# Kernel tuning notes

Hardware: AMD Instinct MI355X
Metric: run time of the kernel (lower is better)

Reference implementation:

```python
import jax, jax.numpy as jnp
import numpy as np

IN, OUT, HID = 64, 32, 256
B, T = 64, 256
NOISE_STD, TAU = 0.05, 0.2


def setup_inputs() -> dict:
    key = jax.random.key(0)
    ks = jax.random.split(key, 8)
    u = jax.random.normal(ks[0], (B, T, IN), dtype=jnp.float32)
    x0 = jax.random.normal(ks[1], (B, HID), dtype=jnp.float32)
    noise = jax.random.normal(ks[2], (T, B, HID), dtype=jnp.float32)
    w_hh_rnn = jax.random.normal(ks[3], (HID, HID), dtype=jnp.float32) * (0.1 / HID ** 0.5)
    w_hh_tbrnn = jax.random.normal(ks[4], (HID, HID, HID), dtype=jnp.float32) * (0.1 / HID)
    w_in_w = jax.random.normal(ks[5], (HID, IN), dtype=jnp.float32)
    w_in_b = jnp.zeros((HID,), dtype=jnp.float32)
    w_out_w = jax.random.normal(ks[6], (OUT, HID), dtype=jnp.float32) * 4.0
    w_out_b = jax.random.normal(ks[7], (OUT,), dtype=jnp.float32) * 0.0
    return {"u": u, "x0": x0, "noise": noise, "w_hh_rnn": w_hh_rnn,
            "w_hh_tbrnn": w_hh_tbrnn, "w_in_w": w_in_w, "w_in_b": w_in_b,
            "w_out_w": w_out_w, "w_out_b": w_out_b}


def reference(u, x0, noise, w_hh_rnn, w_hh_tbrnn, w_in_w, w_in_b, w_out_w, w_out_b):
    # mode='cont', form='rate', adv=False, nonlinearity=tanh, output_nonlinearity=tanh
    u_t_first = jnp.transpose(u, (1, 0, 2))  # [T, B, IN]

    def step(x, inp):
        u_t, n_t = inp
        r = jnp.tanh(x)                                   # rate form
        input_I = u_t @ w_in_w.T + w_in_b                 # [B, HID]
        hidden_W1 = r @ w_hh_rnn.T                        # [B, HID]
        # out[b,j] = sum_{i,k} r[b,i] * W[j,i,k] * r[b,k]
        hidden_W2 = jnp.einsum('bi,jik,bk->bj', r, w_hh_tbrnn, r)
        rec_x = hidden_W1 + hidden_W2 + input_I
        x_new = x + NOISE_STD * n_t + TAU * (-x + rec_x)  # cont mode
        return x_new, x_new

    x_final, traj = jax.lax.scan(step, x0, (u_t_first, noise))
    trajectories = jnp.transpose(traj, (1, 0, 2))         # [B, T, HID]
    output = jnp.tanh(trajectories) @ w_out_w.T + w_out_b  # [B, T, OUT]
    return output, x_final, trajectories
```

## Files before the change

### kernel.cpp

```cpp
#include <hip/hip_runtime.h>
#include <hip/hip_bf16.h>
#include <math.h>

#define HID 256
#define BSZ 64
#define TLEN 256
#define INW 64
#define OUTW 32
#define NOISE_STD 0.05f
#define TAU 0.2f

typedef __attribute__((ext_vector_type(8))) short short8;
typedef __attribute__((ext_vector_type(4))) float floatx4;
typedef unsigned long long u64;

__device__ __forceinline__ int ridx(int b, int k) {
    int P = ((b >> 2) & 7) ^ ((b & 3) << 1);
    return b * 256 + ((((k >> 3) ^ P) & 31) << 3) + (k & 7);
}

__global__ __launch_bounds__(256) void swizzle_kernel(const float* __restrict__ W,
                                                      __hip_bfloat16* __restrict__ Wsw) {
    int g = blockIdx.x * 256 + threadIdx.x;
    int l  = g & 63;
    int ni = (g >> 6) & 15;
    int kk = (g >> 10) & 7;
    int j  = g >> 13;
    int i  = ni * 16 + (l & 15);
    int k0 = kk * 32 + (l >> 4) * 8;
    const float* __restrict__ src = W + ((size_t)j * HID + i) * HID + k0;
    __hip_bfloat16* __restrict__ dst = Wsw + (size_t)g * 8;
#pragma unroll
    for (int e = 0; e < 8; ++e) dst[e] = __float2bfloat16(src[e]);
}

__global__ __launch_bounds__(256) void init_kernel(const float* __restrict__ x0,
                                                   __hip_bfloat16* __restrict__ rT0) {
    int idx = blockIdx.x * 256 + threadIdx.x;
    int b = idx >> 8, k = idx & 255;
    rT0[k * BSZ + b] = __float2bfloat16(tanhf(x0[idx]));
}

__global__ __launch_bounds__(256) void pre_kernel(const float* __restrict__ u,
                                                  const float* __restrict__ w_in_w,
                                                  const float* __restrict__ w_in_b,
                                                  const float* __restrict__ noise,
                                                  float* __restrict__ pre) {
    __shared__ float ulds[BSZ][INW + 4];
    const int t = blockIdx.x;
    const int j = threadIdx.x;
    {
        int b = threadIdx.x >> 2, q = threadIdx.x & 3;
#pragma unroll
        for (int e = 0; e < 4; ++e) {
            float4 v = *(const float4*)(u + ((size_t)b * TLEN + t) * INW + q * 16 + e * 4);
            *(float4*)&ulds[b][q * 16 + e * 4] = v;
        }
    }
    float wreg[INW];
#pragma unroll
    for (int q = 0; q < INW / 4; ++q) {
        float4 v = *(const float4*)(w_in_w + (size_t)j * INW + q * 4);
        wreg[q * 4 + 0] = v.x; wreg[q * 4 + 1] = v.y;
        wreg[q * 4 + 2] = v.z; wreg[q * 4 + 3] = v.w;
    }
    float bias = w_in_b[j];
    __syncthreads();
    for (int b = 0; b < BSZ; ++b) {
        float s = bias;
#pragma unroll
        for (int in_ = 0; in_ < INW; ++in_) s = fmaf(ulds[b][in_], wreg[in_], s);
        float nz = noise[((size_t)t * BSZ + b) * HID + j];
        pre[((size_t)t * HID + j) * BSZ + b] = NOISE_STD * nz + TAU * s;
    }
}

__global__ __launch_bounds__(256, 1) void persist_kernel(
    const __hip_bfloat16* __restrict__ Wsw,
    const float* __restrict__ w_hh,
    const float* __restrict__ u,
    const float* __restrict__ w_in_w,
    const float* __restrict__ w_in_b,
    const float* __restrict__ noise,
    const float* __restrict__ x0,
    u64* __restrict__ rT0,
    u64* __restrict__ rT1,
    float* __restrict__ traj,
    float* __restrict__ trajWS,
    float* __restrict__ xfinal,
    int* __restrict__ ready,
    const float* __restrict__ pre,
    int use_pre, int use_tws) {
    __shared__ short Wlds[65536];
    __shared__ short rlds[16384];

    const int tid  = threadIdx.x;
    const int j    = blockIdx.x;
    const int w    = tid >> 6;
    const int lane = tid & 63;
    const int quad = lane >> 4;
    const int col  = lane & 15;

    float* redw = (float*)rlds;
    __hip_bfloat16* exch = (__hip_bfloat16*)(rlds + 512);
    u64* exchU = (u64*)(rlds + 512);

    {
        const short* __restrict__ src = (const short*)Wsw + (size_t)j * 65536;
#pragma unroll
        for (int m = 0; m < 32; ++m) {
            int i8 = m * 256 + tid;
            *(short8*)&Wlds[i8 * 8] = *(const short8*)&src[(size_t)i8 * 8];
        }
    }
    float whh_reg[4];
#pragma unroll
    for (int nj = 0; nj < 4; ++nj)
        whh_reg[nj] = w_hh[j * HID + (w * 4 + nj) * 16 + col];

    float xb = 0.f;
    if (tid < BSZ) xb = x0[tid * HID + j];
    __syncthreads();

    const int fill_k = tid >> 4;
    const int fill_b0 = (tid & 15) * 4;

#pragma unroll 1
    for (int t = 0; t < TLEN; ++t) {
        if (t > 0) {
            while (__hip_atomic_load(ready + tid * 16, __ATOMIC_RELAXED,
                                     __HIP_MEMORY_SCOPE_AGENT) < t)
                __builtin_amdgcn_s_sleep(1);
            asm volatile("" ::: "memory");
            __syncthreads();
        }

        const u64* __restrict__ rcur = (t & 1) ? rT1 : rT0;
        u64* __restrict__ rnxt = (t & 1) ? rT0 : rT1;

        float extra = 0.f;
        if (tid < BSZ) {
            if (use_pre) {
                extra = pre[((size_t)t * HID + j) * BSZ + tid];
            } else {
                float isum = w_in_b[j];
                const float4* __restrict__ urow =
                    (const float4*)(u + ((size_t)tid * TLEN + t) * INW);
                const float4* __restrict__ wrow = (const float4*)(w_in_w + (size_t)j * INW);
#pragma unroll
                for (int q = 0; q < INW / 4; ++q) {
                    float4 uu = urow[q], ww = wrow[q];
                    isum = fmaf(uu.x, ww.x, isum);
                    isum = fmaf(uu.y, ww.y, isum);
                    isum = fmaf(uu.z, ww.z, isum);
                    isum = fmaf(uu.w, ww.w, isum);
                }
                float nz = noise[((size_t)t * BSZ + tid) * HID + j];
                extra = NOISE_STD * nz + TAU * isum;
            }
        }

        {
            u64 v[16];
#pragma unroll
            for (int c = 0; c < 16; ++c)
                v[c] = __hip_atomic_load(rcur + c * 256 + tid, __ATOMIC_RELAXED,
                                         __HIP_MEMORY_SCOPE_AGENT);
#pragma unroll
            for (int c = 0; c < 16; ++c) {
                int k = c * 16 + fill_k;
#pragma unroll
                for (int i2 = 0; i2 < 4; ++i2)
                    rlds[ridx(fill_b0 + i2, k)] = (short)(v[c] >> (16 * i2));
            }
        }
        __syncthreads();

        floatx4 acc[4][4];
#pragma unroll
        for (int mb = 0; mb < 4; ++mb)
#pragma unroll
            for (int nj = 0; nj < 4; ++nj) acc[mb][nj] = (floatx4){0.f, 0.f, 0.f, 0.f};

#pragma unroll
        for (int kk = 0; kk < 8; ++kk) {
            short8 afrag[4];
#pragma unroll
            for (int mb = 0; mb < 4; ++mb)
                afrag[mb] = *(const short8*)&rlds[ridx(mb * 16 + col, kk * 32 + quad * 8)];
#pragma unroll
            for (int nj = 0; nj < 4; ++nj) {
                short8 bfrag = *(const short8*)&Wlds[((kk * 16 + (w * 4 + nj)) * 64 + lane) * 8];
#pragma unroll
                for (int mb = 0; mb < 4; ++mb)
                    acc[mb][nj] = __builtin_amdgcn_mfma_f32_16x16x32_bf16(
                        afrag[mb], bfrag, acc[mb][nj], 0, 0, 0);
            }
        }

        float part[16];
#pragma unroll
        for (int p = 0; p < 16; ++p) part[p] = 0.f;

#pragma unroll
        for (int nj = 0; nj < 4; ++nj) {
            int i = (w * 4 + nj) * 16 + col;
            float whh = whh_reg[nj];
#pragma unroll
            for (int mb = 0; mb < 4; ++mb) {
#pragma unroll
                for (int reg = 0; reg < 4; ++reg) {
                    int b = mb * 16 + quad * 4 + reg;
                    short rs = rlds[ridx(b, i)];
                    float rv = __bfloat162float(*(__hip_bfloat16*)&rs);
                    part[mb * 4 + reg] = fmaf(rv, acc[mb][nj][reg] + whh, part[mb * 4 + reg]);
                }
            }
        }
#pragma unroll
        for (int s = 1; s < 16; s <<= 1) {
#pragma unroll
            for (int p = 0; p < 16; ++p) part[p] += __shfl_xor(part[p], s, 64);
        }
        __syncthreads();
        if (col == 0) {
#pragma unroll
            for (int mb = 0; mb < 4; ++mb)
#pragma unroll
                for (int reg = 0; reg < 4; ++reg)
                    redw[w * 64 + mb * 16 + quad * 4 + reg] = part[mb * 4 + reg];
        }
        __syncthreads();

        float xn = 0.f;
        if (tid < BSZ) {
            const int b = tid;
            float rec = redw[b] + redw[64 + b] + redw[128 + b] + redw[192 + b];
            xn = xb + extra + TAU * (rec - xb);
            xb = xn;
            if (use_tws) trajWS[((size_t)t * HID + j) * BSZ + b] = xn;
            if (t < TLEN - 1) exch[b] = __float2bfloat16(tanhf(xn));
        }

        if (t < TLEN - 1) {
            if (tid < 16) {
                u64 pv = exchU[tid];
                __hip_atomic_store(rnxt + j * 16 + tid, pv, __ATOMIC_RELAXED,
                                   __HIP_MEMORY_SCOPE_AGENT);
            }
            if (tid < 64)
                asm volatile("s_waitcnt vmcnt(0)" ::: "memory");
            if (tid == 0)
                __hip_atomic_store(ready + j * 16, t + 1, __ATOMIC_RELAXED,
                                   __HIP_MEMORY_SCOPE_AGENT);
        }

        if (!use_tws && tid < BSZ) {
            traj[((size_t)tid * TLEN + t) * HID + j] = xn;
            if (t == TLEN - 1) xfinal[tid * HID + j] = xn;
        }
        if (use_tws && t == TLEN - 1 && tid < BSZ) {
        }
    }
}

__global__ __launch_bounds__(256) void fixup_kernel(
    const float* __restrict__ trajWS,
    const float* __restrict__ w_out_w,
    const float* __restrict__ w_out_b,
    float* __restrict__ traj,
    float* __restrict__ xfinal,
    float* __restrict__ out) {
    __shared__ float xv[BSZ * 257];
    __shared__ float wol[OUTW * 257];
    const int t = blockIdx.x, tid = threadIdx.x;

#pragma unroll
    for (int it = 0; it < 16; ++it) {
        int flat = it * 1024 + tid * 4;
        float4 v = *(const float4*)(trajWS + (size_t)t * 16384 + flat);
        int jj = flat >> 6, b = flat & 63;
        xv[(b + 0) * 257 + jj] = v.x;
        xv[(b + 1) * 257 + jj] = v.y;
        xv[(b + 2) * 257 + jj] = v.z;
        xv[(b + 3) * 257 + jj] = v.w;
    }
#pragma unroll
    for (int it = 0; it < 8; ++it) {
        int flat = it * 1024 + tid * 4;
        float4 v = *(const float4*)(w_out_w + flat);
        int o = flat >> 8, h = flat & 255;
        *(float4*)&wol[o * 257 + h] = v;
    }
    __syncthreads();

    for (int b = 0; b < BSZ; ++b)
        traj[((size_t)b * TLEN + t) * HID + tid] = xv[b * 257 + tid];
    if (t == TLEN - 1)
        for (int b = 0; b < BSZ; ++b)
            xfinal[b * HID + tid] = xv[b * 257 + tid];

    __syncthreads();
#pragma unroll
    for (int it = 0; it < 64; ++it) {
        int b = it;
        xv[b * 257 + tid] = tanhf(xv[b * 257 + tid]);
    }
    __syncthreads();

    const int o = tid & 31;
    const float bias = w_out_b[o];
#pragma unroll 1
    for (int rep = 0; rep < 8; ++rep) {
        int b = rep * 8 + (tid >> 5);
        float s = bias;
#pragma unroll 8
        for (int h = 0; h < HID; ++h)
            s = fmaf(xv[b * 257 + h], wol[o * 257 + h], s);
        out[((size_t)b * TLEN + t) * OUTW + o] = s;
    }
}

__global__ __launch_bounds__(256) void output_kernel(
    const float* __restrict__ traj, const float* __restrict__ w_out_w,
    const float* __restrict__ w_out_b, float* __restrict__ out) {
    __shared__ float th[8][HID + 1];
    const int bt0 = blockIdx.x * 8;
    const int tid = threadIdx.x;
#pragma unroll
    for (int m = 0; m < 8; ++m) {
        int idx = m * 256 + tid;
        th[idx >> 8][idx & 255] = tanhf(traj[(size_t)bt0 * HID + idx]);
    }
    __syncthreads();
    const int row = tid >> 5, o = tid & 31;
    const float* __restrict__ wrow = w_out_w + (size_t)o * HID;
    float s = w_out_b[o];
#pragma unroll 8
    for (int h = 0; h < HID; ++h) s = fmaf(th[row][h], wrow[h], s);
    out[(size_t)(bt0 + row) * OUTW + o] = s;
}

extern "C" void kernel_launch(void* const* d_in, const int* in_sizes, int n_in,
                              void* d_out, int out_size, void* d_ws, size_t ws_size,
                              hipStream_t stream) {
    const float* u       = (const float*)d_in[0];
    const float* x0      = (const float*)d_in[1];
    const float* noise   = (const float*)d_in[2];
    const float* w_hh    = (const float*)d_in[3];
    const float* W       = (const float*)d_in[4];
    const float* w_in_w  = (const float*)d_in[5];
    const float* w_in_b  = (const float*)d_in[6];
    const float* w_out_w = (const float*)d_in[7];
    const float* w_out_b = (const float*)d_in[8];

    float* out    = (float*)d_out;
    float* xfinal = out + (size_t)BSZ * TLEN * OUTW;
    float* traj   = xfinal + (size_t)BSZ * HID;

    char* ws = (char*)d_ws;
    __hip_bfloat16* Wsw = (__hip_bfloat16*)ws;
    u64*   rT0 = (u64*)(ws + 33554432);
    u64*   rT1 = (u64*)(ws + 33587200);
    int*   rdy = (int*)(ws + 33619968);
    float* tws = (float*)(ws + 33636352);
    float* pre = (float*)(ws + 50413568);
    const size_t NEED_TWS = 50413568ull;
    const size_t NEED_PRE = 67190784ull;
    const int use_tws = (ws_size >= NEED_TWS) ? 1 : 0;
    const int use_pre = (ws_size >= NEED_PRE) ? 1 : 0;

    hipMemsetAsync(rdy, 0, 16384, stream);
    swizzle_kernel<<<8192, 256, 0, stream>>>(W, Wsw);
    init_kernel<<<64, 256, 0, stream>>>(x0, (__hip_bfloat16*)rT0);
    if (use_pre)
        pre_kernel<<<TLEN, 256, 0, stream>>>(u, w_in_w, w_in_b, noise, pre);

    persist_kernel<<<256, 256, 0, stream>>>(
        Wsw, w_hh, u, w_in_w, w_in_b, noise, x0,
        rT0, rT1, traj, tws, xfinal, rdy, pre, use_pre, use_tws);

    if (use_tws)
        fixup_kernel<<<TLEN, 256, 0, stream>>>(tws, w_out_w, w_out_b, traj, xfinal, out);
    else
        output_kernel<<<(BSZ * TLEN) / 8, 256, 0, stream>>>(traj, w_out_w, w_out_b, out);
}
```

Baseline: 1.759 ms.

## Replace ready-flag barrier with sequence-tagged data packets and register-resident weights

Drops the separate per-block ready counter and its store/fence/spin handshake. Each exchanged 64-bit word now carries three bf16 rates plus a 16-bit timestep tag, so consumers poll the data itself until every tag matches the current step. The per-block 128KB weight slice also moves from LDS into 32 short8 registers per thread, which frees shared memory but raises register pressure substantially. The tagged scheme relies on each 64-bit atomic store being seen whole; buffer layout and the init kernel change to match the new packet format.

New measurement: 2.848 ms. 1.62x slower.

```diff
diff --git a/kernel.cpp b/kernel.cpp
--- a/kernel.cpp
+++ b/kernel.cpp
@@ -9,6 +9,7 @@
 #define OUTW 32
 #define NOISE_STD 0.05f
 #define TAU 0.2f
+#define NPKT 22
 
 typedef __attribute__((ext_vector_type(8))) short short8;
 typedef __attribute__((ext_vector_type(4))) float floatx4;
@@ -35,10 +36,19 @@
 }
 
 __global__ __launch_bounds__(256) void init_kernel(const float* __restrict__ x0,
-                                                   __hip_bfloat16* __restrict__ rT0) {
-    int idx = blockIdx.x * 256 + threadIdx.x;
-    int b = idx >> 8, k = idx & 255;
-    rT0[k * BSZ + b] = __float2bfloat16(tanhf(x0[idx]));
+                                                   u64* __restrict__ buf0) {
+    int c = blockIdx.x;
+    int k = threadIdx.x;
+    u64 v = 0;
+#pragma unroll
+    for (int e = 0; e < 3; ++e) {
+        int b = 3 * c + e;
+        if (b < BSZ) {
+            __hip_bfloat16 h = __float2bfloat16(tanhf(x0[b * HID + k]));
+            v |= (u64)(*(unsigned short*)&h) << (16 * e);
+        }
+    }
+    buf0[c * 256 + k] = v;
 }
 
 __global__ __launch_bounds__(256) void pre_kernel(const float* __restrict__ u,
@@ -83,16 +93,16 @@
     const float* __restrict__ w_in_b,
     const float* __restrict__ noise,
     const float* __restrict__ x0,
-    u64* __restrict__ rT0,
-    u64* __restrict__ rT1,
+    u64* __restrict__ buf0,
+    u64* __restrict__ buf1,
     float* __restrict__ traj,
     float* __restrict__ trajWS,
     float* __restrict__ xfinal,
-    int* __restrict__ ready,
     const float* __restrict__ pre,
     int use_pre, int use_tws) {
-    __shared__ short Wlds[65536];
     __shared__ short rlds[16384];
+    __shared__ float redw[256];
+    __shared__ __hip_bfloat16 exch[BSZ];
 
     const int tid  = threadIdx.x;
     const int j    = blockIdx.x;
@@ -101,17 +111,15 @@
     const int quad = lane >> 4;
     const int col  = lane & 15;
 
-    float* redw = (float*)rlds;
-    __hip_bfloat16* exch = (__hip_bfloat16*)(rlds + 512);
-    u64* exchU = (u64*)(rlds + 512);
-
+    short8 wreg[32];
     {
-        const short* __restrict__ src = (const short*)Wsw + (size_t)j * 65536;
-#pragma unroll
-        for (int m = 0; m < 32; ++m) {
-            int i8 = m * 256 + tid;
-            *(short8*)&Wlds[i8 * 8] = *(const short8*)&src[(size_t)i8 * 8];
-        }
+        const short* __restrict__ wsh = (const short*)Wsw;
+#pragma unroll
+        for (int kk = 0; kk < 8; ++kk)
+#pragma unroll
+            for (int nj = 0; nj < 4; ++nj)
+                wreg[kk * 4 + nj] = *(const short8*)(wsh +
+                    ((((size_t)j * 8 + kk) * 16 + (w * 4 + nj)) * 64 + lane) * 8);
     }
     float whh_reg[4];
 #pragma unroll
@@ -120,23 +128,11 @@
 
     float xb = 0.f;
     if (tid < BSZ) xb = x0[tid * HID + j];
-    __syncthreads();
-
-    const int fill_k = tid >> 4;
-    const int fill_b0 = (tid & 15) * 4;
 
 #pragma unroll 1
     for (int t = 0; t < TLEN; ++t) {
-        if (t > 0) {
-            while (__hip_atomic_load(ready + tid * 16, __ATOMIC_RELAXED,
-                                     __HIP_MEMORY_SCOPE_AGENT) < t)
-                __builtin_amdgcn_s_sleep(1);
-            asm volatile("" ::: "memory");
-            __syncthreads();
-        }
-
-        const u64* __restrict__ rcur = (t & 1) ? rT1 : rT0;
-        u64* __restrict__ rnxt = (t & 1) ? rT0 : rT1;
+        const u64* __restrict__ rcur = (t & 1) ? buf1 : buf0;
+        u64* __restrict__ rnxt = (t & 1) ? buf0 : buf1;
 
         float extra = 0.f;
         if (tid < BSZ) {
@@ -160,20 +156,30 @@
             }
         }
 
+        u64 v[NPKT];
         {
-            u64 v[16];
-#pragma unroll
-            for (int c = 0; c < 16; ++c)
-                v[c] = __hip_atomic_load(rcur + c * 256 + tid, __ATOMIC_RELAXED,
-                                         __HIP_MEMORY_SCOPE_AGENT);
-#pragma unroll
-            for (int c = 0; c < 16; ++c) {
-                int k = c * 16 + fill_k;
-#pragma unroll
-                for (int i2 = 0; i2 < 4; ++i2)
-                    rlds[ridx(fill_b0 + i2, k)] = (short)(v[c] >> (16 * i2));
+            unsigned need = (1u << NPKT) - 1;
+            while (need) {
+#pragma unroll
+                for (int c = 0; c < NPKT; ++c)
+                    if (need & (1u << c))
+                        v[c] = __hip_atomic_load(rcur + c * 256 + tid, __ATOMIC_RELAXED,
+                                                 __HIP_MEMORY_SCOPE_AGENT);
+#pragma unroll
+                for (int c = 0; c < NPKT; ++c)
+                    if ((need & (1u << c)) && (unsigned)(v[c] >> 48) == (unsigned)t)
+                        need &= ~(1u << c);
+                if (need) __builtin_amdgcn_s_sleep(1);
             }
         }
+        __syncthreads();
+
+#pragma unroll
+        for (int c = 0; c < NPKT - 1; ++c)
+#pragma unroll
+            for (int e = 0; e < 3; ++e)
+                rlds[ridx(3 * c + e, tid)] = (short)(v[c] >> (16 * e));
+        rlds[ridx(63, tid)] = (short)v[NPKT - 1];
         __syncthreads();
 
         floatx4 acc[4][4];
@@ -189,25 +195,22 @@
             for (int mb = 0; mb < 4; ++mb)
                 afrag[mb] = *(const short8*)&rlds[ridx(mb * 16 + col, kk * 32 + quad * 8)];
 #pragma unroll
-            for (int nj = 0; nj < 4; ++nj) {
-                short8 bfrag = *(const short8*)&Wlds[((kk * 16 + (w * 4 + nj)) * 64 + lane) * 8];
+            for (int nj = 0; nj < 4; ++nj)
 #pragma unroll
                 for (int mb = 0; mb < 4; ++mb)
                     acc[mb][nj] = __builtin_amdgcn_mfma_f32_16x16x32_bf16(
-                        afrag[mb], bfrag, acc[mb][nj], 0, 0, 0);
-            }
+                        afrag[mb], wreg[kk * 4 + nj], acc[mb][nj], 0, 0, 0);
         }
 
         float part[16];
 #pragma unroll
         for (int p = 0; p < 16; ++p) part[p] = 0.f;
-
 #pragma unroll
         for (int nj = 0; nj < 4; ++nj) {
             int i = (w * 4 + nj) * 16 + col;
             float whh = whh_reg[nj];
 #pragma unroll
-            for (int mb = 0; mb < 4; ++mb) {
+            for (int mb = 0; mb < 4; ++mb)
 #pragma unroll
                 for (int reg = 0; reg < 4; ++reg) {
                     int b = mb * 16 + quad * 4 + reg;
@@ -215,14 +218,12 @@
                     float rv = __bfloat162float(*(__hip_bfloat16*)&rs);
                     part[mb * 4 + reg] = fmaf(rv, acc[mb][nj][reg] + whh, part[mb * 4 + reg]);
                 }
-            }
         }
 #pragma unroll
         for (int s = 1; s < 16; s <<= 1) {
 #pragma unroll
             for (int p = 0; p < 16; ++p) part[p] += __shfl_xor(part[p], s, 64);
         }
-        __syncthreads();
         if (col == 0) {
 #pragma unroll
             for (int mb = 0; mb < 4; ++mb)
@@ -234,32 +235,28 @@
 
         float xn = 0.f;
         if (tid < BSZ) {
-            const int b = tid;
-            float rec = redw[b] + redw[64 + b] + redw[128 + b] + redw[192 + b];
+            float rec = redw[tid] + redw[64 + tid] + redw[128 + tid] + redw[192 + tid];
             xn = xb + extra + TAU * (rec - xb);
             xb = xn;
-            if (use_tws) trajWS[((size_t)t * HID + j) * BSZ + b] = xn;
-            if (t < TLEN - 1) exch[b] = __float2bfloat16(tanhf(xn));
-        }
-
-        if (t < TLEN - 1) {
-            if (tid < 16) {
-                u64 pv = exchU[tid];
-                __hip_atomic_store(rnxt + j * 16 + tid, pv, __ATOMIC_RELAXED,
-                                   __HIP_MEMORY_SCOPE_AGENT);
+            if (t < TLEN - 1) exch[tid] = __float2bfloat16(tanhf(xn));
+        }
+        if (t < TLEN - 1 && tid < NPKT) {
+            int b0 = 3 * tid;
+            u64 pv = (u64)(unsigned)(t + 1) << 48;
+            pv |= (u64)(*(unsigned short*)&exch[b0]);
+            if (b0 + 1 < BSZ) pv |= (u64)(*(unsigned short*)&exch[b0 + 1]) << 16;
+            if (b0 + 2 < BSZ) pv |= (u64)(*(unsigned short*)&exch[b0 + 2]) << 32;
+            __hip_atomic_store(rnxt + tid * 256 + j, pv, __ATOMIC_RELAXED,
+                               __HIP_MEMORY_SCOPE_AGENT);
+        }
+
+        if (tid < BSZ) {
+            if (use_tws) {
+                trajWS[((size_t)t * HID + j) * BSZ + tid] = xn;
+            } else {
+                traj[((size_t)tid * TLEN + t) * HID + j] = xn;
+                if (t == TLEN - 1) xfinal[tid * HID + j] = xn;
             }
-            if (tid < 64)
-                asm volatile("s_waitcnt vmcnt(0)" ::: "memory");
-            if (tid == 0)
-                __hip_atomic_store(ready + j * 16, t + 1, __ATOMIC_RELAXED,
-                                   __HIP_MEMORY_SCOPE_AGENT);
-        }
-
-        if (!use_tws && tid < BSZ) {
-            traj[((size_t)tid * TLEN + t) * HID + j] = xn;
-            if (t == TLEN - 1) xfinal[tid * HID + j] = xn;
-        }
-        if (use_tws && t == TLEN - 1 && tid < BSZ) {
         }
     }
 }
@@ -302,10 +299,8 @@
 
     __syncthreads();
 #pragma unroll
-    for (int it = 0; it < 64; ++it) {
-        int b = it;
-        xv[b * 257 + tid] = tanhf(xv[b * 257 + tid]);
-    }
+    for (int it = 0; it < 64; ++it)
+        xv[it * 257 + tid] = tanhf(xv[it * 257 + tid]);
     __syncthreads();
 
     const int o = tid & 31;
@@ -360,25 +355,23 @@
 
     char* ws = (char*)d_ws;
     __hip_bfloat16* Wsw = (__hip_bfloat16*)ws;
-    u64*   rT0 = (u64*)(ws + 33554432);
-    u64*   rT1 = (u64*)(ws + 33587200);
-    int*   rdy = (int*)(ws + 33619968);
-    float* tws = (float*)(ws + 33636352);
-    float* pre = (float*)(ws + 50413568);
-    const size_t NEED_TWS = 50413568ull;
-    const size_t NEED_PRE = 67190784ull;
+    u64*   buf0 = (u64*)(ws + 33554432);
+    u64*   buf1 = (u64*)(ws + 33599488);
+    float* tws  = (float*)(ws + 33644544);
+    float* pre  = (float*)(ws + 50421760);
+    const size_t NEED_TWS = 50421760ull;
+    const size_t NEED_PRE = 67198976ull;
     const int use_tws = (ws_size >= NEED_TWS) ? 1 : 0;
     const int use_pre = (ws_size >= NEED_PRE) ? 1 : 0;
 
-    hipMemsetAsync(rdy, 0, 16384, stream);
     swizzle_kernel<<<8192, 256, 0, stream>>>(W, Wsw);
-    init_kernel<<<64, 256, 0, stream>>>(x0, (__hip_bfloat16*)rT0);
+    init_kernel<<<NPKT, 256, 0, stream>>>(x0, buf0);
     if (use_pre)
         pre_kernel<<<TLEN, 256, 0, stream>>>(u, w_in_w, w_in_b, noise, pre);
 
     persist_kernel<<<256, 256, 0, stream>>>(
         Wsw, w_hh, u, w_in_w, w_in_b, noise, x0,
-        rT0, rT1, traj, tws, xfinal, rdy, pre, use_pre, use_tws);
+        buf0, buf1, traj, tws, xfinal, pre, use_pre, use_tws);
 
     if (use_tws)
         fixup_kernel<<<TLEN, 256, 0, stream>>>(tws, w_out_w, w_out_b, traj, xfinal, out);
```
